# Optimization experiments

Hardware: AMD Instinct MI355X
Metric: run time of the kernel (lower is better)

Reference implementation:

```python
import jax, jax.numpy as jnp
import numpy as np

EPS_D = 1e-12  # clamp for sqrt of pairwise distances (diag is exactly 0)


def tr2dist_small(Y):
    # Y: (B, k, N) -> (B, N, N); standard protein-folding coords->distance map
    k = Y.shape[1]
    Z = Y - jnp.mean(Y, axis=2, keepdims=True)
    n2 = jnp.sum(Z * Z, axis=1)                        # (B, N)
    D = n2[:, None, :] + n2[:, :, None] - 2.0 * jnp.einsum('bkn,bkm->bnm', Z, Z)
    D = 3.0 * D / k
    return jnp.sqrt(jnp.maximum(D, EPS_D))


def mean_masked(X, mask, axis, keepdims=True):
    return jnp.sum(X * mask, axis=axis, keepdims=keepdims) / jnp.sum(mask, axis=axis, keepdims=keepdims)


def get_graph_lap(X, mask):
    # X: (B, C, N), mask: (B, 1, N)
    B, C, N = X.shape
    mm = jnp.einsum('bin,bim->bnm', mask, mask)        # (B, N, N) pair mask
    X = X - mean_masked(X, mask, axis=2) * mask
    X = X / jnp.sqrt(jnp.sum(X * X, axis=2, keepdims=True) / jnp.sum(mask, axis=2, keepdims=True) + 1e-4)
    pos = 0.5 * jnp.linspace(0.0, 1.0, N)[None, :] * mask   # (B, 1, N)
    Xa = jnp.concatenate((X, pos), axis=1)
    Wd = tr2dist_small(Xa) * mm
    sigma = mean_masked(Wd, mm, axis=(1, 2))           # (B, 1, 1)
    Wd = jnp.exp(-Wd / sigma * 10.0) * mm
    Wsum = jnp.sum(Wd, axis=1)                         # (B, N)
    L = jnp.zeros_like(Wd) + Wsum[:, :, None] * jnp.eye(N, dtype=Wd.dtype)[None] - Wd
    L = 0.5 * (L + jnp.swapaxes(L, 1, 2))
    return L, Wd


def _forward(Z, mask, K0, Knet, W, Wend):
    h = 0.01
    m = mask[:, None, :]                               # (B, 1, N)
    Z = jnp.tanh(jnp.einsum('oc,bcn->bon', K0, Z)) * m
    nlayers = W.shape[0]
    for i in range(nlayers):
        L, _ = get_graph_lap(Z, m)
        Ki = Knet[i]
        Wi = W[i, :, :, :, 0]                          # (3, C, C) size-1 kernels
        cv = lambda w, x: jnp.einsum('oc,bcn->bon', w, x) * m     # conv1d, k=1
        cvT = lambda w, x: jnp.einsum('co,bcn->bon', w, x) * m    # conv_transpose1d, k=1
        mm1 = lambda x: jnp.einsum('bcn,bnm->bcm', x, L)
        Ai = Ki[0] * cv(Wi[0], Z) + mm1(Ki[1] * cv(Wi[1], Z)) + mm1(mm1(Ki[2] * cv(Wi[2], Z)))
        Ai = (Ai - mean_masked(Ai, m, axis=2)) * m
        Ai = Ai / jnp.sqrt(jnp.sum(Ai * Ai, axis=1, keepdims=True) + 0.001)
        Ai = jax.nn.relu(Ai)
        Ai = Ki[0] * cvT(Wi[0], Ai) + mm1(Ki[1] * cvT(Wi[1], Ai)) + mm1(mm1(Ki[2] * cvT(Wi[2], Ai)))
        Z = Z - h * Ai
    Zout = jnp.einsum('oc,bcn->bon', Wend[:, :, 0], Z) * m       # (B, chan_out, N)
    dists = tuple(tr2dist_small(Zout[:, 3 * i:3 * i + 3, :]) for i in range(Zout.shape[1] // 3))
    return dists + (Zout,)


def setup_inputs() -> dict:
    key = jax.random.key(0)
    ks = jax.random.split(key, 6)
    B, chan_in, chan_out, channels, N, nlayers = 16, 40, 3, 256, 1024, 6
    stdv0 = 0.1 * channels / chan_in
    return {
        'Z': jax.random.normal(ks[0], (B, chan_in, N), dtype=jnp.float32),
        'mask': jnp.ones((B, N), dtype=jnp.float32),
        'K0': jax.random.uniform(ks[1], (channels, chan_in), minval=-stdv0, maxval=stdv0, dtype=jnp.float32),
        'Knet': jax.random.uniform(ks[2], (nlayers, chan_out), minval=-stdv0, maxval=stdv0, dtype=jnp.float32),
        'W': jax.random.uniform(ks[3], (nlayers, 3, channels, channels, 1), minval=-0.1, maxval=0.1, dtype=jnp.float32),
        'Wend': 1e-4 * jax.random.normal(ks[4], (chan_out, channels, 1), dtype=jnp.float32),
    }


def reference(Z, mask, K0, Knet, W, Wend):
    return _forward(Z, mask, K0, Knet, W, Wend)
```

## Files before the change

kernel.cpp:

```cpp
#include <hip/hip_runtime.h>
#include <hip/hip_fp16.h>
#include <math.h>

#define BB 16
#define CIN 40
#define CH 256
#define NN 1024
#define KROWS 257
#define KPAD 288
#define NLAYERS 6

typedef unsigned short ush;
typedef __attribute__((ext_vector_type(8))) short bh8;
typedef __attribute__((ext_vector_type(8))) _Float16 h8;
typedef __attribute__((ext_vector_type(4))) float f4;

__device__ __forceinline__ ush bf16_rne(float x) {
  unsigned int u = __float_as_uint(x);
  u += 0x7fffu + ((u >> 16) & 1u);
  return (ush)(u >> 16);
}
__device__ __forceinline__ float bf16_f(ush h) {
  return __uint_as_float(((unsigned int)h) << 16);
}
__device__ __forceinline__ ush f2h(float x) {
  __half h = __float2half(x);
  return *(ush*)&h;
}
__device__ __forceinline__ float h2f(ush u) {
  __half h = *(__half*)&u;
  return __half2float(h);
}

#define GLD16(gp, lp) __builtin_amdgcn_global_load_lds( \
    (const __attribute__((address_space(1))) void*)(gp), \
    (__attribute__((address_space(3))) void*)(lp), 16, 0, 0)

__device__ __forceinline__ float blockReduceSum(float v) {
  __shared__ float sred[4];
  const int lane = threadIdx.x & 63;
  const int wid  = threadIdx.x >> 6;
  #pragma unroll
  for (int off = 32; off > 0; off >>= 1) v += __shfl_down(v, off, 64);
  __syncthreads();
  if (lane == 0) sred[wid] = v;
  __syncthreads();
  return sred[0] + sred[1] + sred[2] + sred[3];
}

__device__ __forceinline__ void stageA(
    const ush* __restrict__ Ah, const ush* __restrict__ Al, const int sA,
    const ush* __restrict__ Bh, const ush* __restrict__ Bl, const int sB,
    const int kt, ush* buf) {
  const int lane = threadIdx.x & 63;
  const int wid = threadIdx.x >> 6;
  const int srow = lane >> 2;
  const int sl = (lane & 3) ^ ((srow >> 1) & 3);
  #pragma unroll
  for (int cc = 0; cc < 8; cc++) {
    const int c = wid * 8 + cc;
    const ush* src;
    if (c < 8)       src = Ah + (size_t)(c * 16 + srow) * sA + kt + sl * 8;
    else if (c < 16) src = Al + (size_t)((c - 8) * 16 + srow) * sA + kt + sl * 8;
    else if (c < 24) src = Bh + (size_t)((c - 16) * 16 + srow) * sB + kt + sl * 8;
    else             src = Bl + (size_t)((c - 24) * 16 + srow) * sB + kt + sl * 8;
    GLD16(src, buf + c * 512 + lane * 8);
  }
}

__device__ __forceinline__ void computeA(const ush* buf, f4 acc[4][4]) {
  const int lane = threadIdx.x & 63;
  const int wid = threadIdx.x >> 6;
  const int wr = wid >> 1, wc = wid & 1;
  const int frow = lane & 15;
  const int slot8 = (((lane >> 4) ^ ((frow >> 1) & 3)) << 3);
  bh8 ah[4], al[4], bh_[4], bl_[4];
  #pragma unroll
  for (int mi = 0; mi < 4; mi++) {
    const int off = (wr * 64 + mi * 16 + frow) * 32 + slot8;
    ah[mi] = *(const bh8*)&buf[off];
    al[mi] = *(const bh8*)&buf[4096 + off];
  }
  #pragma unroll
  for (int ni = 0; ni < 4; ni++) {
    const int off = (wc * 64 + ni * 16 + frow) * 32 + slot8;
    bh_[ni] = *(const bh8*)&buf[8192 + off];
    bl_[ni] = *(const bh8*)&buf[12288 + off];
  }
  #pragma unroll
  for (int mi = 0; mi < 4; mi++)
    #pragma unroll
    for (int ni = 0; ni < 4; ni++) {
      acc[mi][ni] = __builtin_amdgcn_mfma_f32_16x16x32_bf16(ah[mi], bh_[ni], acc[mi][ni], 0, 0, 0);
      acc[mi][ni] = __builtin_amdgcn_mfma_f32_16x16x32_bf16(ah[mi], bl_[ni], acc[mi][ni], 0, 0, 0);
      acc[mi][ni] = __builtin_amdgcn_mfma_f32_16x16x32_bf16(al[mi], bh_[ni], acc[mi][ni], 0, 0, 0);
    }
}

__device__ __forceinline__ void stageCV(
    const ush* __restrict__ Ap, const int sA,
    const ush* __restrict__ Bh, const ush* __restrict__ Bl, const int sB,
    const int kt, ush* buf) {
  const int lane = threadIdx.x & 63;
  const int wid = threadIdx.x >> 6;
  const int srow = lane >> 2;
  const int sl = (lane & 3) ^ ((srow >> 1) & 3);
  #pragma unroll
  for (int cc = 0; cc < 6; cc++) {
    const int c = wid * 6 + cc;
    const ush* src;
    if (c < 8)       src = Ap + (size_t)(c * 16 + srow) * sA + kt + sl * 8;
    else if (c < 16) src = Bh + (size_t)((c - 8) * 16 + srow) * sB + kt + sl * 8;
    else             src = Bl + (size_t)((c - 16) * 16 + srow) * sB + kt + sl * 8;
    GLD16(src, buf + c * 512 + lane * 8);
  }
}

__device__ __forceinline__ void computeCV(const ush* buf, f4 acc[4][4]) {
  const int lane = threadIdx.x & 63;
  const int wid = threadIdx.x >> 6;
  const int wr = wid >> 1, wc = wid & 1;
  const int frow = lane & 15;
  const int slot8 = (((lane >> 4) ^ ((frow >> 1) & 3)) << 3);
  h8 a_[4], bh_[4], bl_[4];
  #pragma unroll
  for (int mi = 0; mi < 4; mi++) {
    const int off = (wr * 64 + mi * 16 + frow) * 32 + slot8;
    a_[mi] = *(const h8*)&buf[off];
  }
  #pragma unroll
  for (int ni = 0; ni < 4; ni++) {
    const int off = (wc * 64 + ni * 16 + frow) * 32 + slot8;
    bh_[ni] = *(const h8*)&buf[4096 + off];
    bl_[ni] = *(const h8*)&buf[8192 + off];
  }
  #pragma unroll
  for (int mi = 0; mi < 4; mi++)
    #pragma unroll
    for (int ni = 0; ni < 4; ni++) {
      acc[mi][ni] = __builtin_amdgcn_mfma_f32_16x16x32_f16(a_[mi], bh_[ni], acc[mi][ni], 0, 0, 0);
      acc[mi][ni] = __builtin_amdgcn_mfma_f32_16x16x32_f16(a_[mi], bl_[ni], acc[mi][ni], 0, 0, 0);
    }
}

__device__ __forceinline__ void stageMM(
    const ush* __restrict__ Ah, const ush* __restrict__ Al, const int sA,
    const ush* __restrict__ Bp, const int sB, const int kt, ush* buf) {
  const int lane = threadIdx.x & 63;
  const int wid = threadIdx.x >> 6;
  const int srow = lane >> 2;
  const int sl = (lane & 3) ^ ((srow >> 1) & 3);
  #pragma unroll
  for (int cc = 0; cc < 4; cc++) {
    const int c = wid * 4 + cc;
    const ush* src;
    if (c < 4)       src = Ah + (size_t)(c * 16 + srow) * sA + kt + sl * 8;
    else if (c < 8)  src = Al + (size_t)((c - 4) * 16 + srow) * sA + kt + sl * 8;
    else             src = Bp + (size_t)((c - 8) * 16 + srow) * sB + kt + sl * 8;
    GLD16(src, buf + c * 512 + lane * 8);
  }
}

__device__ __forceinline__ void computeMM(const ush* buf, f4 acc[4][2]) {
  const int lane = threadIdx.x & 63;
  const int wid = threadIdx.x >> 6;
  const int frow = lane & 15;
  const int slot8 = (((lane >> 4) ^ ((frow >> 1) & 3)) << 3);
  h8 ah[4], al[4], b_[2];
  #pragma unroll
  for (int mi = 0; mi < 4; mi++) {
    const int off = (mi * 16 + frow) * 32 + slot8;
    ah[mi] = *(const h8*)&buf[off];
    al[mi] = *(const h8*)&buf[2048 + off];
  }
  #pragma unroll
  for (int ni = 0; ni < 2; ni++) {
    const int off = (wid * 32 + ni * 16 + frow) * 32 + slot8;
    b_[ni] = *(const h8*)&buf[4096 + off];
  }
  #pragma unroll
  for (int mi = 0; mi < 4; mi++)
    #pragma unroll
    for (int ni = 0; ni < 2; ni++) {
      acc[mi][ni] = __builtin_amdgcn_mfma_f32_16x16x32_f16(ah[mi], b_[ni], acc[mi][ni], 0, 0, 0);
      acc[mi][ni] = __builtin_amdgcn_mfma_f32_16x16x32_f16(al[mi], b_[ni], acc[mi][ni], 0, 0, 0);
    }
}

__global__ void k0_kernel(const float* __restrict__ Zin, const float* __restrict__ K0,
                          const float* __restrict__ mask, float* __restrict__ Zc,
                          float* __restrict__ statS1, float* __restrict__ statS2) {
  const int b = blockIdx.y;
  const int o = blockIdx.x;
  __shared__ float w[CIN];
  if (threadIdx.x < CIN) w[threadIdx.x] = K0[o * CIN + threadIdx.x];
  __syncthreads();
  float s1 = 0.f, s2 = 0.f;
  for (int n = threadIdx.x; n < NN; n += 256) {
    float acc = 0.f;
    #pragma unroll
    for (int c = 0; c < CIN; c++) acc += w[c] * Zin[((size_t)b * CIN + c) * NN + n];
    const float z = tanhf(acc) * mask[b * NN + n];
    Zc[((size_t)b * CH + o) * NN + n] = z;
    s1 += z; s2 += z * z;
  }
  s1 = blockReduceSum(s1);
  s2 = blockReduceSum(s2);
  if (threadIdx.x == 0) {
    const size_t base = ((size_t)b * CH + o) * 8;
    statS1[base] = s1; statS2[base] = s2;
    #pragma unroll
    for (int k = 1; k < 8; k++) { statS1[base + k] = 0.f; statS2[base + k] = 0.f; }
  }
}

__global__ void masksum_kernel(const float* __restrict__ mask, float* __restrict__ msum,
                               float* __restrict__ pmpos) {
  const int b = blockIdx.x;
  float v = 0.f, p = 0.f;
  for (int n = threadIdx.x; n < NN; n += 256) {
    const float m = mask[b * NN + n];
    v += m;
    p += 0.5f * ((float)n * (1.0f / (NN - 1))) * m;
  }
  v = blockReduceSum(v);
  p = blockReduceSum(p);
  if (threadIdx.x == 0) { msum[b] = v; pmpos[b] = p * (1.0f / NN); }
}

__global__ void wprep_kernel(const float* __restrict__ W, ush* __restrict__ Wm,
                             ush* __restrict__ Wt) {
  __shared__ float t[64][65];
  const int mat = blockIdx.y;
  const int ty = blockIdx.x >> 2, tx = blockIdx.x & 3;
  const float* src = W + (size_t)mat * CH * CH;
  const int tid = threadIdx.x;
  const int lr = tid >> 2;
  const int lc = (tid & 3) * 16;
  float v[16];
  #pragma unroll
  for (int j = 0; j < 16; j += 4)
    *(float4*)&v[j] = *(const float4*)&src[(size_t)(ty * 64 + lr) * CH + tx * 64 + lc + j];
  ush hv[16];
  #pragma unroll
  for (int j = 0; j < 16; j++) {
    hv[j] = f2h(v[j]);
    t[lr][lc + j] = v[j];
  }
  const size_t offm = (size_t)mat * CH * CH + (size_t)(ty * 64 + lr) * CH + tx * 64 + lc;
  #pragma unroll
  for (int j = 0; j < 16; j += 4)
    *(ushort4*)&Wm[offm + j] = *(ushort4*)&hv[j];
  __syncthreads();
  #pragma unroll
  for (int j = 0; j < 16; j++) hv[j] = f2h(t[lc + j][lr]);
  const size_t offt = (size_t)mat * CH * CH + (size_t)(tx * 64 + lr) * CH + ty * 64 + lc;
  #pragma unroll
  for (int j = 0; j < 16; j += 4)
    *(ushort4*)&Wt[offt + j] = *(ushort4*)&hv[j];
}

__global__ void rowstatZ_kernel(const float* __restrict__ statS1, const float* __restrict__ statS2,
                                const float* __restrict__ msum, float* __restrict__ muZ,
                                float* __restrict__ rsZ) {
  const int b = blockIdx.x;
  const int c = threadIdx.x;
  const size_t base = ((size_t)b * CH + c) * 8;
  float S1 = 0.f, S2 = 0.f;
  #pragma unroll
  for (int k = 0; k < 8; k++) { S1 += statS1[base + k]; S2 += statS2[base + k]; }
  const float M = msum[b];
  const float mu = S1 / M;
  const float q = fmaxf(S2 - mu * S1, 0.f);
  muZ[b * CH + c] = mu;
  rsZ[b * CH + c] = 1.0f / sqrtf(q / M + 1e-4f);
}

__global__ void rowstatU_kernel(const float* __restrict__ statS1, const float* __restrict__ msum,
                                float* __restrict__ rmean) {
  const int b = blockIdx.x;
  const int c = threadIdx.x;
  const size_t base = ((size_t)b * CH + c) * 8;
  float S1 = 0.f;
  #pragma unroll
  for (int k = 0; k < 8; k++) S1 += statS1[base + k];
  rmean[b * CH + c] = S1 / msum[b];
}

__global__ void tsplitZ_kernel(const float* __restrict__ in, ush* __restrict__ Th,
                               ush* __restrict__ Tl) {
  __shared__ float t[32][65];
  const int b = blockIdx.z;
  const int n0 = blockIdx.x * 64;
  const int k0 = blockIdx.y * 32;
  const float* src = in + (size_t)b * CH * NN;
  const int tid = threadIdx.x;
  const int lr = tid >> 3;
  const int lc = (tid & 7) * 8;
  const int gk = k0 + lr;
  *(float4*)&t[lr][lc]     = *(const float4*)&src[(size_t)gk * NN + n0 + lc];
  *(float4*)&t[lr][lc + 4] = *(const float4*)&src[(size_t)gk * NN + n0 + lc + 4];
  __syncthreads();
  const int on = tid >> 2;
  const int ok = (tid & 3) * 8;
  ush hv[8], lv[8];
  #pragma unroll
  for (int j = 0; j < 8; j++) {
    const float v = t[ok + j][on];
    hv[j] = f2h(v); lv[j] = f2h(v - h2f(hv[j]));
  }
  const size_t off = ((size_t)b * NN + n0 + on) * CH + k0 + ok;
  *(ushort4*)&Th[off] = *(ushort4*)&hv[0];
  *(ushort4*)&Th[off + 4] = *(ushort4*)&hv[4];
  *(ushort4*)&Tl[off] = *(ushort4*)&lv[0];
  *(ushort4*)&Tl[off + 4] = *(ushort4*)&lv[4];
}

__global__ void tsplitY2_kernel(const ush* __restrict__ Zsh, const ush* __restrict__ Zsl,
                                const float* __restrict__ mask, const float* __restrict__ muZ,
                                const float* __restrict__ rsZ, const float* __restrict__ pmpos,
                                ush* __restrict__ Th, ush* __restrict__ Tl,
                                float* __restrict__ n2part) {
  const int b = blockIdx.z;
  const int n0 = blockIdx.x * 64;
  const int k0 = blockIdx.y * 32;
  const int tid = threadIdx.x;
  const int n = n0 + (tid >> 2);
  const int kc = k0 + (tid & 3) * 8;
  const float mn = mask[b * NN + n];
  float val[8];
  if (kc + 7 < CH) {
    const size_t zoff = ((size_t)b * NN + n) * CH + kc;
    const ushort4 h0 = *(const ushort4*)&Zsh[zoff];
    const ushort4 h1 = *(const ushort4*)&Zsh[zoff + 4];
    const ushort4 l0 = *(const ushort4*)&Zsl[zoff];
    const ushort4 l1 = *(const ushort4*)&Zsl[zoff + 4];
    const float4 mu0 = *(const float4*)&muZ[b * CH + kc];
    const float4 mu1 = *(const float4*)&muZ[b * CH + kc + 4];
    const float4 rs0 = *(const float4*)&rsZ[b * CH + kc];
    const float4 rs1 = *(const float4*)&rsZ[b * CH + kc + 4];
    val[0] = (h2f(h0.x) + h2f(l0.x) - mu0.x * mn) * rs0.x;
    val[1] = (h2f(h0.y) + h2f(l0.y) - mu0.y * mn) * rs0.y;
    val[2] = (h2f(h0.z) + h2f(l0.z) - mu0.z * mn) * rs0.z;
    val[3] = (h2f(h0.w) + h2f(l0.w) - mu0.w * mn) * rs0.w;
    val[4] = (h2f(h1.x) + h2f(l1.x) - mu1.x * mn) * rs1.x;
    val[5] = (h2f(h1.y) + h2f(l1.y) - mu1.y * mn) * rs1.y;
    val[6] = (h2f(h1.z) + h2f(l1.z) - mu1.z * mn) * rs1.z;
    val[7] = (h2f(h1.w) + h2f(l1.w) - mu1.w * mn) * rs1.w;
  } else {
    #pragma unroll
    for (int j = 0; j < 8; j++) {
      const int gk = kc + j;
      val[j] = (gk == CH) ? (0.5f * ((float)n * (1.0f / (NN - 1))) * mn - pmpos[b]) : 0.f;
    }
  }
  float s = 0.f;
  ush hv[8], lv[8];
  #pragma unroll
  for (int j = 0; j < 8; j++) {
    s += val[j] * val[j];
    hv[j] = bf16_rne(val[j]);
    lv[j] = bf16_rne(val[j] - bf16_f(hv[j]));
  }
  const size_t off = ((size_t)b * NN + n) * KPAD + kc;
  *(ushort4*)&Th[off] = *(ushort4*)&hv[0];
  *(ushort4*)&Th[off + 4] = *(ushort4*)&hv[4];
  *(ushort4*)&Tl[off] = *(ushort4*)&lv[0];
  *(ushort4*)&Tl[off + 4] = *(ushort4*)&lv[4];
  s += __shfl_xor(s, 1, 64);
  s += __shfl_xor(s, 2, 64);
  if ((tid & 3) == 0) n2part[((size_t)b * 9 + blockIdx.y) * NN + n] = s;
}

__global__ void n2red_kernel(const float* __restrict__ n2part, float* __restrict__ n2) {
  const int idx = blockIdx.x * 256 + threadIdx.x;
  const int b = idx >> 10, n = idx & 1023;
  float s = 0.f;
  #pragma unroll
  for (int kb = 0; kb < 9; kb++) s += n2part[((size_t)b * 9 + kb) * NN + n];
  n2[idx] = s;
}

__global__ __launch_bounds__(256, 2)
void gram_v4_kernel(const ush* __restrict__ Yth, const ush* __restrict__ Ytl,
                    const float* __restrict__ n2, const float* __restrict__ mask,
                    ush* __restrict__ Dp, float* __restrict__ sigpart) {
  __shared__ ush lds[32768];
  const int bid = blockIdx.x;
  const int logical = (bid & 7) * 72 + (bid >> 3);
  const int b = logical / 36;
  int t = logical - b * 36;
  int ty = 0;
  while (t >= 8 - ty) { t -= 8 - ty; ++ty; }
  const int tx = ty + t;
  const int i0 = ty * 128;
  const int j0 = tx * 128;
  const ush* Ah = Yth + (size_t)b * NN * KPAD + (size_t)i0 * KPAD;
  const ush* Al = Ytl + (size_t)b * NN * KPAD + (size_t)i0 * KPAD;
  const ush* Bh = Yth + (size_t)b * NN * KPAD + (size_t)j0 * KPAD;
  const ush* Bl = Ytl + (size_t)b * NN * KPAD + (size_t)j0 * KPAD;
  f4 acc[4][4];
  const f4 z4 = {0.f, 0.f, 0.f, 0.f};
  #pragma unroll
  for (int mi = 0; mi < 4; mi++)
    #pragma unroll
    for (int ni = 0; ni < 4; ni++) acc[mi][ni] = z4;
  stageA(Ah, Al, KPAD, Bh, Bl, KPAD, 0, lds);
  __syncthreads();
  int pb = 0;
  for (int kt = 32; kt < KPAD; kt += 32) {
    stageA(Ah, Al, KPAD, Bh, Bl, KPAD, kt, lds + (pb ^ 1) * 16384);
    computeA(lds + pb * 16384, acc);
    __syncthreads();
    pb ^= 1;
  }
  computeA(lds + pb * 16384, acc);
  const int lane = threadIdx.x & 63;
  const int wid = threadIdx.x >> 6;
  const int wr = wid >> 1, wc = wid & 1;
  const int frow = lane & 15, hh = lane >> 4;
  const float scale = 3.0f / 257.0f;
  float lsum = 0.f;
  #pragma unroll
  for (int ni = 0; ni < 4; ni++) {
    const int jl = wc * 64 + ni * 16 + frow;
    const int j = j0 + jl;
    const float n2j = n2[b * NN + j];
    const float mkj = mask[b * NN + j];
    #pragma unroll
    for (int mi = 0; mi < 4; mi++) {
      const int il = wr * 64 + mi * 16 + hh * 4;
      ush dv[4];
      #pragma unroll
      for (int r = 0; r < 4; r++) {
        const int i = i0 + il + r;
        const float D = scale * (n2[b * NN + i] + n2j - 2.0f * acc[mi][ni][r]);
        const float d = sqrtf(fmaxf(D, 1e-12f));
        const float mmv = mask[b * NN + i] * mkj;
        const float wd = d * mmv;
        lsum += wd * mmv;
        dv[r] = f2h(wd);
      }
      if (ty != tx) {
        uint2 mr;
        mr.x = (unsigned)dv[0] | ((unsigned)dv[1] << 16);
        mr.y = (unsigned)dv[2] | ((unsigned)dv[3] << 16);
        *(uint2*)&Dp[((size_t)b * NN + j) * NN + i0 + il] = mr;
      }
      #pragma unroll
      for (int r = 0; r < 4; r++) {
        const unsigned v = dv[r];
        const unsigned vp = (unsigned)__shfl_xor((int)v, 1, 64);
        if ((frow & 1) == 0)
          *(unsigned*)&Dp[((size_t)b * NN + i0 + il + r) * NN + j] = v | (vp << 16);
      }
    }
  }
  if (ty != tx) lsum *= 2.0f;
  #pragma unroll
  for (int off = 32; off > 0; off >>= 1) lsum += __shfl_down(lsum, off, 64);
  __syncthreads();
  float* rbuf = (float*)lds;
  if (lane == 0) rbuf[wid] = lsum;
  __syncthreads();
  if (threadIdx.x == 0)
    sigpart[(size_t)b * 64 + ty * 8 + tx] = rbuf[0] + rbuf[1] + rbuf[2] + rbuf[3];
}

__global__ void sigfinal_kernel(const float* __restrict__ sigpart, const float* __restrict__ msum,
                                float* __restrict__ fbuf) {
  const int b = blockIdx.x;
  float v = 0.f;
  if (threadIdx.x < 64) {
    const int ty = threadIdx.x >> 3, tx = threadIdx.x & 7;
    if (ty <= tx) v = sigpart[b * 64 + threadIdx.x];
  }
  v = blockReduceSum(v);
  if (threadIdx.x == 0) { const float ms = msum[b]; fbuf[b] = -10.0f * ms * ms / v; }
}

__global__ void expw3_kernel(const ush* __restrict__ Dp, const float* __restrict__ mask,
                             const float* __restrict__ fbuf, ush* __restrict__ Wp) {
  const int b = blockIdx.y, n = blockIdx.x;
  const float fb = fbuf[b];
  const float mn = mask[b * NN + n];
  const size_t roff = ((size_t)b * NN + n) * NN;
  const int t = threadIdx.x;
  const float4 mk = ((const float4*)(mask + b * NN))[t];
  const ushort4 dp = *(const ushort4*)&Dp[roff + t * 4];
  const float w0 = expf(fb * h2f(dp.x)) * mn * mk.x;
  const float w1 = expf(fb * h2f(dp.y)) * mn * mk.y;
  const float w2 = expf(fb * h2f(dp.z)) * mn * mk.z;
  const float w3 = expf(fb * h2f(dp.w)) * mn * mk.w;
  const float s = blockReduceSum(w0 + w1 + w2 + w3);
  float v0 = -w0, v1 = -w1, v2 = -w2, v3 = -w3;
  if ((n >> 2) == t) {
    const int r = n & 3;
    if (r == 0) v0 += s; else if (r == 1) v1 += s; else if (r == 2) v2 += s; else v3 += s;
  }
  ushort4 h4;
  h4.x = f2h(v0); h4.y = f2h(v1); h4.z = f2h(v2); h4.w = f2h(v3);
  *(ushort4*)&Wp[roff + t * 4] = h4;
}

__global__ __launch_bounds__(256, 2)
void cvall_kernel(const ush* __restrict__ Ap, const ush* __restrict__ Bth,
                  const ush* __restrict__ Btl, const float* __restrict__ mask,
                  const float* __restrict__ Kis, unsigned int* __restrict__ Cpack,
                  ush* __restrict__ C2h, ush* __restrict__ C2l) {
  __shared__ ush lds[32768];
  const int bid = blockIdx.x;
  const int logical = (bid & 7) * 96 + (bid >> 3);
  const int b = logical / 48;
  const int inner = logical - b * 48;
  const int c0g = inner & 7;
  const int r0g = inner >> 3;
  const int r0 = r0g * 128;
  const int c0 = c0g * 128;
  const ush* Aq = Ap + (size_t)r0 * CH;
  const ush* Bh = Bth + (size_t)b * NN * CH + (size_t)c0 * CH;
  const ush* Bl = Btl + (size_t)b * NN * CH + (size_t)c0 * CH;
  f4 acc[4][4];
  const f4 z4 = {0.f, 0.f, 0.f, 0.f};
  #pragma unroll
  for (int mi = 0; mi < 4; mi++)
    #pragma unroll
    for (int ni = 0; ni < 4; ni++) acc[mi][ni] = z4;
  stageCV(Aq, CH, Bh, Bl, CH, 0, lds);
  __syncthreads();
  int pb = 0;
  for (int kt = 32; kt < CH; kt += 32) {
    stageCV(Aq, CH, Bh, Bl, CH, kt, lds + (pb ^ 1) * 12288);
    computeCV(lds + pb * 12288, acc);
    __syncthreads();
    pb ^= 1;
  }
  computeCV(lds + pb * 12288, acc);
  __syncthreads();
  unsigned int* tl = (unsigned int*)lds;
  const int lane = threadIdx.x & 63;
  const int wid = threadIdx.x >> 6;
  const int wr = wid >> 1, wc = wid & 1;
  const int frow = lane & 15, hh = lane >> 4;
  const float alpha = Kis[r0g >> 1];
  #pragma unroll
  for (int ni = 0; ni < 4; ni++) {
    const int jl = wc * 64 + ni * 16 + frow;
    const float am = alpha * mask[b * NN + c0 + jl];
    #pragma unroll
    for (int mi = 0; mi < 4; mi++) {
      const int il = wr * 64 + mi * 16 + hh * 4;
      unsigned int pv[4];
      #pragma unroll
      for (int r = 0; r < 4; r++) {
        const float v = acc[mi][ni][r] * am;
        const ush h = f2h(v);
        const ush l = f2h(v - h2f(h));
        pv[r] = (unsigned int)h | ((unsigned int)l << 16);
      }
      const int slot = (il >> 2) ^ (jl & 31);
      *(uint4*)&tl[jl * 128 + slot * 4] = *(uint4*)pv;
    }
  }
  __syncthreads();
  const int rrow = threadIdx.x >> 1;
  const int rch = (threadIdx.x & 1) * 64;
  if (r0g < 4) {
    unsigned int* dst = Cpack + ((size_t)b * 512 + r0 + rrow) * NN + c0 + rch;
    #pragma unroll
    for (int g = 0; g < 16; g++) {
      unsigned int pw[4];
      #pragma unroll
      for (int q = 0; q < 4; q++) {
        const int jl = rch + g * 4 + q;
        const int slot = (rrow >> 2) ^ (jl & 31);
        pw[q] = tl[jl * 128 + slot * 4 + (rrow & 3)];
      }
      *(uint4*)&dst[g * 4] = *(uint4*)pw;
    }
  } else {
    const size_t obase = ((size_t)b * 256 + (r0 - 512) + rrow) * NN + c0 + rch;
    #pragma unroll
    for (int g = 0; g < 8; g++) {
      unsigned int hw[4], lw[4];
      #pragma unroll
      for (int q = 0; q < 4; q++) {
        unsigned int h2[2], l2[2];
        #pragma unroll
        for (int e = 0; e < 2; e++) {
          const int jl = rch + g * 8 + q * 2 + e;
          const int slot = (rrow >> 2) ^ (jl & 31);
          const unsigned int v = tl[jl * 128 + slot * 4 + (rrow & 3)];
          h2[e] = v & 0xffffu; l2[e] = v >> 16;
        }
        hw[q] = h2[0] | (h2[1] << 16);
        lw[q] = l2[0] | (l2[1] << 16);
      }
      *(uint4*)&C2h[obase + g * 8] = *(uint4*)hw;
      *(uint4*)&C2l[obase + g * 8] = *(uint4*)lw;
    }
  }
}

template <int OUTMODE, int STATS>
__global__ __launch_bounds__(256, 3)
void mm1_v6_kernel(const ush* __restrict__ Xh, const ush* __restrict__ Xl, const size_t xStride,
                   const ush* __restrict__ Wp,
                   const unsigned int* __restrict__ addp, const size_t aStride,
                   const float* __restrict__ zin, const float* __restrict__ mask,
                   float* __restrict__ outF, ush* __restrict__ outH, ush* __restrict__ outL,
                   float* __restrict__ statS1, float* __restrict__ statS2) {
  __shared__ ush lds[16384];
  const int bid = blockIdx.x;
  const int logical = (bid & 7) * 64 + (bid >> 3);
  const int b = logical >> 5;
  const int inner = logical & 31;
  const int n0 = (inner & 7) * 128;
  const int r0 = (inner >> 3) * 64;
  const ush* Ah = Xh + (size_t)b * xStride + (size_t)r0 * NN;
  const ush* Al = Xl + (size_t)b * xStride + (size_t)r0 * NN;
  const ush* Bp = Wp + (size_t)b * NN * NN + (size_t)n0 * NN;
  f4 acc[4][2];
  const f4 z4 = {0.f, 0.f, 0.f, 0.f};
  #pragma unroll
  for (int mi = 0; mi < 4; mi++) { acc[mi][0] = z4; acc[mi][1] = z4; }
  stageMM(Ah, Al, NN, Bp, NN, 0, lds);
  __syncthreads();
  int pb = 0;
  for (int kt = 32; kt < NN; kt += 32) {
    stageMM(Ah, Al, NN, Bp, NN, kt, lds + (pb ^ 1) * 8192);
    computeMM(lds + pb * 8192, acc);
    __syncthreads();
    pb ^= 1;
  }
  computeMM(lds + pb * 8192, acc);
  const int lane = threadIdx.x & 63;
  const int wid = threadIdx.x >> 6;
  const int frow = lane & 15, hh = lane >> 4;
  float a1[4][4];
  float a2[4][4];
  if (STATS) {
    #pragma unroll
    for (int mi = 0; mi < 4; mi++)
      #pragma unroll
      for (int r = 0; r < 4; r++) { a1[mi][r] = 0.f; a2[mi][r] = 0.f; }
  }
  __syncthreads();
  unsigned int* tl = (unsigned int*)lds;
  #pragma unroll
  for (int ni = 0; ni < 2; ni++) {
    const int jl = wid * 32 + ni * 16 + frow;
    const int col = n0 + jl;
    const float mk = STATS ? mask[b * NN + col] : 0.f;
    #pragma unroll
    for (int mi = 0; mi < 4; mi++) {
      const int il = mi * 16 + hh * 4;
      unsigned int pv[4];
      #pragma unroll
      for (int r = 0; r < 4; r++) {
        const int row = r0 + il + r;
        const unsigned int av = addp[(size_t)b * aStride + (size_t)row * NN + col];
        const float o = acc[mi][ni][r] + h2f((ush)(av & 0xffffu)) + h2f((ush)(av >> 16));
        float val;
        if (OUTMODE == 2) {
          const size_t ooff = (size_t)b * CH * NN + (size_t)row * NN + col;
          val = zin[ooff] - 0.01f * o;
          outF[ooff] = val;
        } else {
          val = o;
        }
        if (STATS) { a1[mi][r] += val * mk; a2[mi][r] += val * val * mk; }
        const ush h = f2h(val);
        const ush l = f2h(val - h2f(h));
        pv[r] = (unsigned int)h | ((unsigned int)l << 16);
      }
      const int slot = (il >> 2) ^ (jl & 15);
      *(uint4*)&tl[jl * 64 + slot * 4] = *(uint4*)pv;
    }
  }
  __syncthreads();
  if (OUTMODE == 0) {
    const int rrow = threadIdx.x >> 2;
    const int rch = (threadIdx.x & 3) * 32;
    const size_t obase = ((size_t)b * 256 + r0 + rrow) * NN + n0 + rch;
    #pragma unroll
    for (int g = 0; g < 4; g++) {
      unsigned int hw[4], lw[4];
      #pragma unroll
      for (int q = 0; q < 4; q++) {
        unsigned int h2[2], l2[2];
        #pragma unroll
        for (int e = 0; e < 2; e++) {
          const int jl = rch + g * 8 + q * 2 + e;
          const int slot = (rrow >> 2) ^ (jl & 15);
          const unsigned int v = tl[jl * 64 + slot * 4 + (rrow & 3)];
          h2[e] = v & 0xffffu; l2[e] = v >> 16;
        }
        hw[q] = h2[0] | (h2[1] << 16);
        lw[q] = l2[0] | (l2[1] << 16);
      }
      *(uint4*)&outH[obase + g * 8] = *(uint4*)hw;
      *(uint4*)&outL[obase + g * 8] = *(uint4*)lw;
    }
  } else {
    const int nloc = threadIdx.x >> 1;
    const int ch0 = (threadIdx.x & 1) * 32;
    #pragma unroll
    for (int half = 0; half < 2; half++) {
      unsigned int hw[8], lw[8];
      #pragma unroll
      for (int q = 0; q < 8; q++) {
        const int ila = ch0 + half * 16 + q * 2;
        const int ilb = ila + 1;
        const unsigned int va = tl[nloc * 64 + (((ila >> 2) ^ (nloc & 15)) << 2) + (ila & 3)];
        const unsigned int vb = tl[nloc * 64 + (((ilb >> 2) ^ (nloc & 15)) << 2) + (ilb & 3)];
        hw[q] = (va & 0xffffu) | (vb << 16);
        lw[q] = (va >> 16) | (vb & 0xffff0000u);
      }
      const size_t zoff = ((size_t)b * NN + n0 + nloc) * CH + r0 + ch0 + half * 16;
      *(uint4*)&outH[zoff] = *(uint4*)&hw[0];
      *(uint4*)&outH[zoff + 8] = *(uint4*)&hw[4];
      *(uint4*)&outL[zoff] = *(uint4*)&lw[0];
      *(uint4*)&outL[zoff + 8] = *(uint4*)&lw[4];
    }
  }
  if (STATS) {
    #pragma unroll
    for (int mi = 0; mi < 4; mi++)
      #pragma unroll
      for (int r = 0; r < 4; r++) {
        #pragma unroll
        for (int d = 1; d < 16; d <<= 1) {
          a1[mi][r] += __shfl_xor(a1[mi][r], d, 64);
          a2[mi][r] += __shfl_xor(a2[mi][r], d, 64);
        }
      }
    __syncthreads();
    float* s1b = (float*)lds;
    float* s2b = s1b + 256;
    if (frow == 0) {
      #pragma unroll
      for (int mi = 0; mi < 4; mi++)
        #pragma unroll
        for (int r = 0; r < 4; r++) {
          const int row = mi * 16 + hh * 4 + r;
          s1b[wid * 64 + row] = a1[mi][r];
          s2b[wid * 64 + row] = a2[mi][r];
        }
    }
    __syncthreads();
    if (threadIdx.x < 64) {
      const int row = threadIdx.x;
      const float p1 = s1b[row] + s1b[64 + row] + s1b[128 + row] + s1b[192 + row];
      const float p2 = s2b[row] + s2b[64 + row] + s2b[128 + row] + s2b[192 + row];
      const int nblk = n0 >> 7;
      statS1[((size_t)b * CH + r0 + row) * 8 + nblk] = p1;
      statS2[((size_t)b * CH + r0 + row) * 8 + nblk] = p2;
    }
  }
}

__global__ void csq_kernel(const ush* __restrict__ Uh, const ush* __restrict__ Ul,
                           const float* __restrict__ mask, const float* __restrict__ rmean,
                           float* __restrict__ part) {
  const int b = blockIdx.y, cc = blockIdx.x;
  const int n = threadIdx.x * 4;
  const float4 m4 = *(const float4*)&mask[b * NN + n];
  float4 s4 = {0.f, 0.f, 0.f, 0.f};
  for (int r = 0; r < 16; r++) {
    const int c = cc * 16 + r;
    const float rm = rmean[b * CH + c];
    const size_t uoff = ((size_t)b * 256 + c) * NN + n;
    const ushort4 uh = *(const ushort4*)&Uh[uoff];
    const ushort4 ul = *(const ushort4*)&Ul[uoff];
    float a;
    a = (h2f(uh.x) + h2f(ul.x) - rm) * m4.x; s4.x += a * a;
    a = (h2f(uh.y) + h2f(ul.y) - rm) * m4.y; s4.y += a * a;
    a = (h2f(uh.z) + h2f(ul.z) - rm) * m4.z; s4.z += a * a;
    a = (h2f(uh.w) + h2f(ul.w) - rm) * m4.w; s4.w += a * a;
  }
  *(float4*)&part[((size_t)(b * 16 + cc)) * NN + n] = s4;
}

__global__ void csq2_kernel(const float* __restrict__ part, float* __restrict__ rs) {
  const int b = blockIdx.y;
  const int n = blockIdx.x * 256 + threadIdx.x;
  float s = 0.001f;
  #pragma unroll
  for (int cc = 0; cc < 16; cc++) s += part[((size_t)(b * 16 + cc)) * NN + n];
  rs[b * NN + n] = 1.0f / sqrtf(s);
}

__global__ void tsplitN2_kernel(const ush* __restrict__ Uh, const ush* __restrict__ Ul,
                                const float* __restrict__ mask, const float* __restrict__ rmean,
                                const float* __restrict__ rs, ush* __restrict__ Th,
                                ush* __restrict__ Tl) {
  __shared__ float t[32][65];
  const int b = blockIdx.z;
  const int n0 = blockIdx.x * 64;
  const int k0 = blockIdx.y * 32;
  const int tid = threadIdx.x;
  const int lr = tid >> 3;
  const int lc = (tid & 7) * 8;
  const int gc = k0 + lr;
  const float rm = rmean[b * CH + gc];
  const float4 ma = *(const float4*)&mask[b * NN + n0 + lc];
  const float4 mb = *(const float4*)&mask[b * NN + n0 + lc + 4];
  const float4 ra = *(const float4*)&rs[b * NN + n0 + lc];
  const float4 rb = *(const float4*)&rs[b * NN + n0 + lc + 4];
  const size_t uoff = ((size_t)b * 256 + gc) * NN + n0 + lc;
  const ushort4 ha = *(const ushort4*)&Uh[uoff];
  const ushort4 hb = *(const ushort4*)&Uh[uoff + 4];
  const ushort4 la = *(const ushort4*)&Ul[uoff];
  const ushort4 lb = *(const ushort4*)&Ul[uoff + 4];
  t[lr][lc + 0] = fmaxf((h2f(ha.x) + h2f(la.x) - rm) * ma.x * ra.x, 0.f);
  t[lr][lc + 1] = fmaxf((h2f(ha.y) + h2f(la.y) - rm) * ma.y * ra.y, 0.f);
  t[lr][lc + 2] = fmaxf((h2f(ha.z) + h2f(la.z) - rm) * ma.z * ra.z, 0.f);
  t[lr][lc + 3] = fmaxf((h2f(ha.w) + h2f(la.w) - rm) * ma.w * ra.w, 0.f);
  t[lr][lc + 4] = fmaxf((h2f(hb.x) + h2f(lb.x) - rm) * mb.x * rb.x, 0.f);
  t[lr][lc + 5] = fmaxf((h2f(hb.y) + h2f(lb.y) - rm) * mb.y * rb.y, 0.f);
  t[lr][lc + 6] = fmaxf((h2f(hb.z) + h2f(lb.z) - rm) * mb.z * rb.z, 0.f);
  t[lr][lc + 7] = fmaxf((h2f(hb.w) + h2f(lb.w) - rm) * mb.w * rb.w, 0.f);
  __syncthreads();
  const int on = tid >> 2;
  const int ok = (tid & 3) * 8;
  ush hv[8], lv[8];
  #pragma unroll
  for (int j = 0; j < 8; j++) {
    const float v = t[ok + j][on];
    hv[j] = f2h(v); lv[j] = f2h(v - h2f(hv[j]));
  }
  const size_t off = ((size_t)b * NN + n0 + on) * CH + k0 + ok;
  *(ushort4*)&Th[off] = *(ushort4*)&hv[0];
  *(ushort4*)&Th[off + 4] = *(ushort4*)&hv[4];
  *(ushort4*)&Tl[off] = *(ushort4*)&lv[0];
  *(ushort4*)&Tl[off + 4] = *(ushort4*)&lv[4];
}

__global__ void zout_kernel(const float* __restrict__ Z, const float* __restrict__ Wend,
                            const float* __restrict__ mask, float* __restrict__ outZ,
                            float* __restrict__ Zcent) {
  const int b = blockIdx.x;
  __shared__ float w[3 * CH];
  for (int i = threadIdx.x; i < 3 * CH; i += 256) w[i] = Wend[i];
  __syncthreads();
  float a[3][4];
  #pragma unroll
  for (int j = 0; j < 4; j++) { a[0][j] = 0.f; a[1][j] = 0.f; a[2][j] = 0.f; }
  const float* Zb = Z + (size_t)b * CH * NN;
  for (int c = 0; c < CH; c++) {
    const float w0 = w[c], w1 = w[CH + c], w2 = w[2 * CH + c];
    #pragma unroll
    for (int j = 0; j < 4; j++) {
      float zv = Zb[(size_t)c * NN + threadIdx.x + j * 256];
      a[0][j] += w0 * zv; a[1][j] += w1 * zv; a[2][j] += w2 * zv;
    }
  }
  float sum[3] = {0.f, 0.f, 0.f};
  #pragma unroll
  for (int j = 0; j < 4; j++) {
    const int n = threadIdx.x + j * 256;
    const float mv = mask[b * NN + n];
    #pragma unroll
    for (int o = 0; o < 3; o++) {
      a[o][j] *= mv;
      outZ[((size_t)b * 3 + o) * NN + n] = a[o][j];
      sum[o] += a[o][j];
    }
  }
  for (int o = 0; o < 3; o++) {
    float s = blockReduceSum(sum[o]);
    const float mean = s * (1.0f / NN);
    #pragma unroll
    for (int j = 0; j < 4; j++) {
      const int n = threadIdx.x + j * 256;
      Zcent[((size_t)b * 3 + o) * NN + n] = a[o][j] - mean;
    }
  }
}

__global__ void dist_kernel(const float* __restrict__ Zcent, float* __restrict__ outD) {
  const int b = blockIdx.z;
  const int n = blockIdx.y;
  const int m = blockIdx.x * 256 + threadIdx.x;
  const float* Zb = Zcent + (size_t)b * 3 * NN;
  const float x0 = Zb[n], x1 = Zb[NN + n], x2 = Zb[2 * NN + n];
  const float d0 = x0 - Zb[m], d1 = x1 - Zb[NN + m], d2 = x2 - Zb[2 * NN + m];
  const float D = d0 * d0 + d1 * d1 + d2 * d2;
  outD[((size_t)b * NN + n) * NN + m] = sqrtf(fmaxf(D, 1e-12f));
}

extern "C" void kernel_launch(void* const* d_in, const int* in_sizes, int n_in,
                              void* d_out, int out_size, void* d_ws, size_t ws_size,
                              hipStream_t stream) {
  const float* Zin  = (const float*)d_in[0];
  const float* mask = (const float*)d_in[1];
  const float* K0   = (const float*)d_in[2];
  const float* Knet = (const float*)d_in[3];
  const float* W    = (const float*)d_in[4];
  const float* Wend = (const float*)d_in[5];
  float* out = (float*)d_out;

  ush* Wp = (ush*)out;
  ush* Dp = Wp + (size_t)BB * NN * NN;
  float* outZ = out + (size_t)BB * NN * NN;

  float* p = (float*)d_ws;
  float* uni = p; p += (size_t)BB * 768 * NN;
  ush* Yth = (ush*)uni;
  ush* Ytl = Yth + (size_t)BB * NN * KPAD;
  unsigned int* Cpack = (unsigned int*)uni;
  ush* C2h = (ush*)(uni + (size_t)BB * 512 * NN);
  ush* C2l = C2h + (size_t)BB * 256 * NN;

  float* Zcur = p; p += (size_t)BB * CH * NN;
  ush* Thb = (ush*)p; p += (size_t)BB * NN * CH / 2;
  ush* Tlb = (ush*)p; p += (size_t)BB * NN * CH / 2;
  ush* Zsh = (ush*)p; p += (size_t)BB * NN * CH / 2;
  ush* Zsl = (ush*)p; p += (size_t)BB * NN * CH / 2;
  ush* Wm = (ush*)p; p += (size_t)18 * CH * CH / 2;
  ush* Wt = (ush*)p; p += (size_t)18 * CH * CH / 2;
  float* n2b   = p; p += BB * NN;
  float* rsb   = p; p += BB * NN;
  float* msum  = p; p += BB;
  float* pmpos = p; p += BB;
  float* sigp  = p; p += BB * 64;
  float* fbuf  = p; p += BB;
  float* rmeanb= p; p += BB * CH;
  float* muZ   = p; p += BB * CH;
  float* rsZ   = p; p += BB * CH;
  float* statS1= p; p += (size_t)BB * CH * 8;
  float* statS2= p; p += (size_t)BB * CH * 8;
  float* n2part= p; p += (size_t)BB * 9 * NN;
  float* partb = p; p += (size_t)BB * 16 * NN;
  float* Zcent = p; p += BB * 3 * NN;

  const dim3 gtsZ(NN / 64, CH / 32, BB);
  const dim3 gtsY(NN / 64, KPAD / 32, BB);
  const size_t sC = (size_t)512 * NN;
  const size_t sT = (size_t)CH * NN;

  masksum_kernel<<<BB, 256, 0, stream>>>(mask, msum, pmpos);
  wprep_kernel<<<dim3(16, 18), 256, 0, stream>>>(W, Wm, Wt);
  k0_kernel<<<dim3(CH, BB), 256, 0, stream>>>(Zin, K0, mask, Zcur, statS1, statS2);
  tsplitZ_kernel<<<gtsZ, 256, 0, stream>>>(Zcur, Zsh, Zsl);

  for (int layer = 0; layer < NLAYERS; layer++) {
    rowstatZ_kernel<<<BB, 256, 0, stream>>>(statS1, statS2, msum, muZ, rsZ);
    tsplitY2_kernel<<<gtsY, 256, 0, stream>>>(Zsh, Zsl, mask, muZ, rsZ, pmpos, Yth, Ytl, n2part);
    n2red_kernel<<<BB * NN / 256, 256, 0, stream>>>(n2part, n2b);
    gram_v4_kernel<<<576, 256, 0, stream>>>(Yth, Ytl, n2b, mask, Dp, sigp);
    sigfinal_kernel<<<BB, 256, 0, stream>>>(sigp, msum, fbuf);
    expw3_kernel<<<dim3(NN, BB), 256, 0, stream>>>(Dp, mask, fbuf, Wp);

    const ush* Am = Wm + (size_t)layer * 3 * CH * CH;
    const ush* At = Wt + (size_t)layer * 3 * CH * CH;
    const float* Ki = Knet + layer * 3;

    cvall_kernel<<<768, 256, 0, stream>>>(Am, Zsh, Zsl, mask, Ki, Cpack, C2h, C2l);
    mm1_v6_kernel<0, 0><<<512, 256, 0, stream>>>(C2h, C2l, sT, Wp,
        Cpack + (size_t)256 * NN, sC, nullptr, nullptr, nullptr, Thb, Tlb, nullptr, nullptr);
    mm1_v6_kernel<0, 1><<<512, 256, 0, stream>>>(Thb, Tlb, sT, Wp,
        Cpack, sC, nullptr, mask, nullptr, C2h, C2l, statS1, statS2);

    rowstatU_kernel<<<BB, 256, 0, stream>>>(statS1, msum, rmeanb);
    csq_kernel<<<dim3(16, BB), 256, 0, stream>>>(C2h, C2l, mask, rmeanb, partb);
    csq2_kernel<<<dim3(NN / 256, BB), 256, 0, stream>>>(partb, rsb);
    tsplitN2_kernel<<<gtsZ, 256, 0, stream>>>(C2h, C2l, mask, rmeanb, rsb, Thb, Tlb);

    cvall_kernel<<<768, 256, 0, stream>>>(At, Thb, Tlb, mask, Ki, Cpack, C2h, C2l);
    mm1_v6_kernel<0, 0><<<512, 256, 0, stream>>>(C2h, C2l, sT, Wp,
        Cpack + (size_t)256 * NN, sC, nullptr, nullptr, nullptr, Thb, Tlb, nullptr, nullptr);
    mm1_v6_kernel<2, 1><<<512, 256, 0, stream>>>(Thb, Tlb, sT, Wp,
        Cpack, sC, Zcur, mask, Zcur, Zsh, Zsl, statS1, statS2);
  }

  zout_kernel<<<BB, 256, 0, stream>>>(Zcur, Wend, mask, outZ, Zcent);
  dist_kernel<<<dim3(NN / 256, NN, BB), 256, 0, stream>>>(Zcent, out);
}
```

Measured before the change: 1.806 ms.

## Fold position channel into gram epilogue and write cvall outputs directly

The 257th channel (the position feature) is removed from the padded K dimension of the gram GEMM. Its contribution is added as a rank-1 term in the epilogue using a precomputed per-node position vector, so the GEMM K loop drops from 288 to 256. Separately, cvall no longer transposes its outputs through LDS; it pairs lanes with a shuffle and writes to global directly, which lets LDS shrink and raises occupancy hints for cvall and mm1. The trade-off is that the direct stores are narrower and less coalesced than the old staged writes.

```diff
diff --git a/kernel.cpp b/kernel.cpp
--- a/kernel.cpp
+++ b/kernel.cpp
@@ -6,8 +6,6 @@
 #define CIN 40
 #define CH 256
 #define NN 1024
-#define KROWS 257
-#define KPAD 288
 #define NLAYERS 6
 
 typedef unsigned short ush;
@@ -215,7 +213,7 @@
 }
 
 __global__ void masksum_kernel(const float* __restrict__ mask, float* __restrict__ msum,
-                               float* __restrict__ pmpos) {
+                               float* __restrict__ posv) {
   const int b = blockIdx.x;
   float v = 0.f, p = 0.f;
   for (int n = threadIdx.x; n < NN; n += 256) {
@@ -225,7 +223,10 @@
   }
   v = blockReduceSum(v);
   p = blockReduceSum(p);
-  if (threadIdx.x == 0) { msum[b] = v; pmpos[b] = p * (1.0f / NN); }
+  const float pm = p * (1.0f / NN);
+  if (threadIdx.x == 0) msum[b] = v;
+  for (int n = threadIdx.x; n < NN; n += 256)
+    posv[b * NN + n] = 0.5f * ((float)n * (1.0f / (NN - 1))) * mask[b * NN + n] - pm;
 }
 
 __global__ void wprep_kernel(const float* __restrict__ W, ush* __restrict__ Wm,
@@ -318,9 +319,8 @@
 
 __global__ void tsplitY2_kernel(const ush* __restrict__ Zsh, const ush* __restrict__ Zsl,
                                 const float* __restrict__ mask, const float* __restrict__ muZ,
-                                const float* __restrict__ rsZ, const float* __restrict__ pmpos,
-                                ush* __restrict__ Th, ush* __restrict__ Tl,
-                                float* __restrict__ n2part) {
+                                const float* __restrict__ rsZ, ush* __restrict__ Th,
+                                ush* __restrict__ Tl, float* __restrict__ n2part) {
   const int b = blockIdx.z;
   const int n0 = blockIdx.x * 64;
   const int k0 = blockIdx.y * 32;
@@ -328,32 +328,24 @@
   const int n = n0 + (tid >> 2);
   const int kc = k0 + (tid & 3) * 8;
   const float mn = mask[b * NN + n];
+  const size_t zoff = ((size_t)b * NN + n) * CH + kc;
+  const ushort4 h0 = *(const ushort4*)&Zsh[zoff];
+  const ushort4 h1 = *(const ushort4*)&Zsh[zoff + 4];
+  const ushort4 l0 = *(const ushort4*)&Zsl[zoff];
+  const ushort4 l1 = *(const ushort4*)&Zsl[zoff + 4];
+  const float4 mu0 = *(const float4*)&muZ[b * CH + kc];
+  const float4 mu1 = *(const float4*)&muZ[b * CH + kc + 4];
+  const float4 rs0 = *(const float4*)&rsZ[b * CH + kc];
+  const float4 rs1 = *(const float4*)&rsZ[b * CH + kc + 4];
   float val[8];
-  if (kc + 7 < CH) {
-    const size_t zoff = ((size_t)b * NN + n) * CH + kc;
-    const ushort4 h0 = *(const ushort4*)&Zsh[zoff];
-    const ushort4 h1 = *(const ushort4*)&Zsh[zoff + 4];
-    const ushort4 l0 = *(const ushort4*)&Zsl[zoff];
-    const ushort4 l1 = *(const ushort4*)&Zsl[zoff + 4];
-    const float4 mu0 = *(const float4*)&muZ[b * CH + kc];
-    const float4 mu1 = *(const float4*)&muZ[b * CH + kc + 4];
-    const float4 rs0 = *(const float4*)&rsZ[b * CH + kc];
-    const float4 rs1 = *(const float4*)&rsZ[b * CH + kc + 4];
-    val[0] = (h2f(h0.x) + h2f(l0.x) - mu0.x * mn) * rs0.x;
-    val[1] = (h2f(h0.y) + h2f(l0.y) - mu0.y * mn) * rs0.y;
-    val[2] = (h2f(h0.z) + h2f(l0.z) - mu0.z * mn) * rs0.z;
-    val[3] = (h2f(h0.w) + h2f(l0.w) - mu0.w * mn) * rs0.w;
-    val[4] = (h2f(h1.x) + h2f(l1.x) - mu1.x * mn) * rs1.x;
-    val[5] = (h2f(h1.y) + h2f(l1.y) - mu1.y * mn) * rs1.y;
-    val[6] = (h2f(h1.z) + h2f(l1.z) - mu1.z * mn) * rs1.z;
-    val[7] = (h2f(h1.w) + h2f(l1.w) - mu1.w * mn) * rs1.w;
-  } else {
-    #pragma unroll
-    for (int j = 0; j < 8; j++) {
-      const int gk = kc + j;
-      val[j] = (gk == CH) ? (0.5f * ((float)n * (1.0f / (NN - 1))) * mn - pmpos[b]) : 0.f;
-    }
-  }
+  val[0] = (h2f(h0.x) + h2f(l0.x) - mu0.x * mn) * rs0.x;
+  val[1] = (h2f(h0.y) + h2f(l0.y) - mu0.y * mn) * rs0.y;
+  val[2] = (h2f(h0.z) + h2f(l0.z) - mu0.z * mn) * rs0.z;
+  val[3] = (h2f(h0.w) + h2f(l0.w) - mu0.w * mn) * rs0.w;
+  val[4] = (h2f(h1.x) + h2f(l1.x) - mu1.x * mn) * rs1.x;
+  val[5] = (h2f(h1.y) + h2f(l1.y) - mu1.y * mn) * rs1.y;
+  val[6] = (h2f(h1.z) + h2f(l1.z) - mu1.z * mn) * rs1.z;
+  val[7] = (h2f(h1.w) + h2f(l1.w) - mu1.w * mn) * rs1.w;
   float s = 0.f;
   ush hv[8], lv[8];
   #pragma unroll
@@ -362,29 +354,32 @@
     hv[j] = bf16_rne(val[j]);
     lv[j] = bf16_rne(val[j] - bf16_f(hv[j]));
   }
-  const size_t off = ((size_t)b * NN + n) * KPAD + kc;
+  const size_t off = ((size_t)b * NN + n) * CH + kc;
   *(ushort4*)&Th[off] = *(ushort4*)&hv[0];
   *(ushort4*)&Th[off + 4] = *(ushort4*)&hv[4];
   *(ushort4*)&Tl[off] = *(ushort4*)&lv[0];
   *(ushort4*)&Tl[off + 4] = *(ushort4*)&lv[4];
   s += __shfl_xor(s, 1, 64);
   s += __shfl_xor(s, 2, 64);
-  if ((tid & 3) == 0) n2part[((size_t)b * 9 + blockIdx.y) * NN + n] = s;
-}
-
-__global__ void n2red_kernel(const float* __restrict__ n2part, float* __restrict__ n2) {
+  if ((tid & 3) == 0) n2part[((size_t)b * 8 + blockIdx.y) * NN + n] = s;
+}
+
+__global__ void n2red_kernel(const float* __restrict__ n2part, const float* __restrict__ posv,
+                             float* __restrict__ n2) {
   const int idx = blockIdx.x * 256 + threadIdx.x;
-  const int b = idx >> 10, n = idx & 1023;
-  float s = 0.f;
-  #pragma unroll
-  for (int kb = 0; kb < 9; kb++) s += n2part[((size_t)b * 9 + kb) * NN + n];
+  const int b = idx >> 10;
+  const float pv = posv[idx];
+  float s = pv * pv;
+  #pragma unroll
+  for (int kb = 0; kb < 8; kb++) s += n2part[((size_t)b * 8 + kb) * NN + (idx & 1023)];
   n2[idx] = s;
 }
 
 __global__ __launch_bounds__(256, 2)
-void gram_v4_kernel(const ush* __restrict__ Yth, const ush* __restrict__ Ytl,
+void gram_v5_kernel(const ush* __restrict__ Yth, const ush* __restrict__ Ytl,
                     const float* __restrict__ n2, const float* __restrict__ mask,
-                    ush* __restrict__ Dp, float* __restrict__ sigpart) {
+                    const float* __restrict__ posv, ush* __restrict__ Dp,
+                    float* __restrict__ sigpart) {
   __shared__ ush lds[32768];
   const int bid = blockIdx.x;
   const int logical = (bid & 7) * 72 + (bid >> 3);
@@ -395,21 +390,21 @@
   const int tx = ty + t;
   const int i0 = ty * 128;
   const int j0 = tx * 128;
-  const ush* Ah = Yth + (size_t)b * NN * KPAD + (size_t)i0 * KPAD;
-  const ush* Al = Ytl + (size_t)b * NN * KPAD + (size_t)i0 * KPAD;
-  const ush* Bh = Yth + (size_t)b * NN * KPAD + (size_t)j0 * KPAD;
-  const ush* Bl = Ytl + (size_t)b * NN * KPAD + (size_t)j0 * KPAD;
+  const ush* Ah = Yth + (size_t)b * NN * CH + (size_t)i0 * CH;
+  const ush* Al = Ytl + (size_t)b * NN * CH + (size_t)i0 * CH;
+  const ush* Bh = Yth + (size_t)b * NN * CH + (size_t)j0 * CH;
+  const ush* Bl = Ytl + (size_t)b * NN * CH + (size_t)j0 * CH;
   f4 acc[4][4];
   const f4 z4 = {0.f, 0.f, 0.f, 0.f};
   #pragma unroll
   for (int mi = 0; mi < 4; mi++)
     #pragma unroll
     for (int ni = 0; ni < 4; ni++) acc[mi][ni] = z4;
-  stageA(Ah, Al, KPAD, Bh, Bl, KPAD, 0, lds);
+  stageA(Ah, Al, CH, Bh, Bl, CH, 0, lds);
   __syncthreads();
   int pb = 0;
-  for (int kt = 32; kt < KPAD; kt += 32) {
-    stageA(Ah, Al, KPAD, Bh, Bl, KPAD, kt, lds + (pb ^ 1) * 16384);
+  for (int kt = 32; kt < CH; kt += 32) {
+    stageA(Ah, Al, CH, Bh, Bl, CH, kt, lds + (pb ^ 1) * 16384);
     computeA(lds + pb * 16384, acc);
     __syncthreads();
     pb ^= 1;
@@ -427,6 +422,7 @@
     const int j = j0 + jl;
     const float n2j = n2[b * NN + j];
     const float mkj = mask[b * NN + j];
+    const float pj = posv[b * NN + j];
     #pragma unroll
     for (int mi = 0; mi < 4; mi++) {
       const int il = wr * 64 + mi * 16 + hh * 4;
@@ -434,7 +430,8 @@
       #pragma unroll
       for (int r = 0; r < 4; r++) {
         const int i = i0 + il + r;
-        const float D = scale * (n2[b * NN + i] + n2j - 2.0f * acc[mi][ni][r]);
+        const float g = acc[mi][ni][r] + posv[b * NN + i] * pj;
+        const float D = scale * (n2[b * NN + i] + n2j - 2.0f * g);
         const float d = sqrtf(fmaxf(D, 1e-12f));
         const float mmv = mask[b * NN + i] * mkj;
         const float wd = d * mmv;
@@ -503,12 +500,12 @@
   *(ushort4*)&Wp[roff + t * 4] = h4;
 }
 
-__global__ __launch_bounds__(256, 2)
+__global__ __launch_bounds__(256, 3)
 void cvall_kernel(const ush* __restrict__ Ap, const ush* __restrict__ Bth,
                   const ush* __restrict__ Btl, const float* __restrict__ mask,
                   const float* __restrict__ Kis, unsigned int* __restrict__ Cpack,
                   ush* __restrict__ C2h, ush* __restrict__ C2l) {
-  __shared__ ush lds[32768];
+  __shared__ ush lds[24576];
   const int bid = blockIdx.x;
   const int logical = (bid & 7) * 96 + (bid >> 3);
   const int b = logical / 48;
@@ -536,8 +533,6 @@
     pb ^= 1;
   }
   computeCV(lds + pb * 12288, acc);
-  __syncthreads();
-  unsigned int* tl = (unsigned int*)lds;
   const int lane = threadIdx.x & 63;
   const int wid = threadIdx.x >> 6;
   const int wr = wid >> 1, wc = wid & 1;
@@ -546,64 +541,38 @@
   #pragma unroll
   for (int ni = 0; ni < 4; ni++) {
     const int jl = wc * 64 + ni * 16 + frow;
-    const float am = alpha * mask[b * NN + c0 + jl];
+    const int col = c0 + jl;
+    const float am = alpha * mask[b * NN + col];
     #pragma unroll
     for (int mi = 0; mi < 4; mi++) {
       const int il = wr * 64 + mi * 16 + hh * 4;
-      unsigned int pv[4];
       #pragma unroll
       for (int r = 0; r < 4; r++) {
+        const int row = r0 + il + r;
         const float v = acc[mi][ni][r] * am;
         const ush h = f2h(v);
         const ush l = f2h(v - h2f(h));
-        pv[r] = (unsigned int)h | ((unsigned int)l << 16);
+        const unsigned pv = (unsigned)h | ((unsigned)l << 16);
+        const unsigned pvp = (unsigned)__shfl_xor((int)pv, 1, 64);
+        if ((frow & 1) == 0) {
+          if (r0g < 4) {
+            uint2 w2; w2.x = pv; w2.y = pvp;
+            *(uint2*)&Cpack[((size_t)b * 512 + row) * NN + col] = w2;
+          } else {
+            const size_t obase = ((size_t)b * 256 + (row - 512)) * NN + col;
+            const unsigned hw = (pv & 0xffffu) | (pvp << 16);
+            const unsigned lw = (pv >> 16) | (pvp & 0xffff0000u);
+            *(unsigned*)&C2h[obase] = hw;
+            *(unsigned*)&C2l[obase] = lw;
+          }
+        }
       }
-      const int slot = (il >> 2) ^ (jl & 31);
-      *(uint4*)&tl[jl * 128 + slot * 4] = *(uint4*)pv;
-    }
-  }
-  __syncthreads();
-  const int rrow = threadIdx.x >> 1;
-  const int rch = (threadIdx.x & 1) * 64;
-  if (r0g < 4) {
-    unsigned int* dst = Cpack + ((size_t)b * 512 + r0 + rrow) * NN + c0 + rch;
-    #pragma unroll
-    for (int g = 0; g < 16; g++) {
-      unsigned int pw[4];
-      #pragma unroll
-      for (int q = 0; q < 4; q++) {
-        const int jl = rch + g * 4 + q;
-        const int slot = (rrow >> 2) ^ (jl & 31);
-        pw[q] = tl[jl * 128 + slot * 4 + (rrow & 3)];
-      }
-      *(uint4*)&dst[g * 4] = *(uint4*)pw;
-    }
-  } else {
-    const size_t obase = ((size_t)b * 256 + (r0 - 512) + rrow) * NN + c0 + rch;
-    #pragma unroll
-    for (int g = 0; g < 8; g++) {
-      unsigned int hw[4], lw[4];
-      #pragma unroll
-      for (int q = 0; q < 4; q++) {
-        unsigned int h2[2], l2[2];
-        #pragma unroll
-        for (int e = 0; e < 2; e++) {
-          const int jl = rch + g * 8 + q * 2 + e;
-          const int slot = (rrow >> 2) ^ (jl & 31);
-          const unsigned int v = tl[jl * 128 + slot * 4 + (rrow & 3)];
-          h2[e] = v & 0xffffu; l2[e] = v >> 16;
-        }
-        hw[q] = h2[0] | (h2[1] << 16);
-        lw[q] = l2[0] | (l2[1] << 16);
-      }
-      *(uint4*)&C2h[obase + g * 8] = *(uint4*)hw;
-      *(uint4*)&C2l[obase + g * 8] = *(uint4*)lw;
     }
   }
 }
 
 template <int OUTMODE, int STATS>
-__global__ __launch_bounds__(256, 3)
+__global__ __launch_bounds__(256, 5)
 void mm1_v6_kernel(const ush* __restrict__ Xh, const ush* __restrict__ Xl, const size_t xStride,
                    const ush* __restrict__ Wp,
                    const unsigned int* __restrict__ addp, const size_t aStride,
@@ -908,7 +877,7 @@
   float* p = (float*)d_ws;
   float* uni = p; p += (size_t)BB * 768 * NN;
   ush* Yth = (ush*)uni;
-  ush* Ytl = Yth + (size_t)BB * NN * KPAD;
+  ush* Ytl = Yth + (size_t)BB * NN * CH;
   unsigned int* Cpack = (unsigned int*)uni;
   ush* C2h = (ush*)(uni + (size_t)BB * 512 * NN);
   ush* C2l = C2h + (size_t)BB * 256 * NN;
@@ -923,7 +892,7 @@
   float* n2b   = p; p += BB * NN;
   float* rsb   = p; p += BB * NN;
   float* msum  = p; p += BB;
-  float* pmpos = p; p += BB;
+  float* posv  = p; p += BB * NN;
   float* sigp  = p; p += BB * 64;
   float* fbuf  = p; p += BB;
   float* rmeanb= p; p += BB * CH;
@@ -931,25 +900,24 @@
   float* rsZ   = p; p += BB * CH;
   float* statS1= p; p += (size_t)BB * CH * 8;
   float* statS2= p; p += (size_t)BB * CH * 8;
-  float* n2part= p; p += (size_t)BB * 9 * NN;
+  float* n2part= p; p += (size_t)BB * 8 * NN;
   float* partb = p; p += (size_t)BB * 16 * NN;
   float* Zcent = p; p += BB * 3 * NN;
 
   const dim3 gtsZ(NN / 64, CH / 32, BB);
-  const dim3 gtsY(NN / 64, KPAD / 32, BB);
   const size_t sC = (size_t)512 * NN;
   const size_t sT = (size_t)CH * NN;
 
-  masksum_kernel<<<BB, 256, 0, stream>>>(mask, msum, pmpos);
+  masksum_kernel<<<BB, 256, 0, stream>>>(mask, msum, posv);
   wprep_kernel<<<dim3(16, 18), 256, 0, stream>>>(W, Wm, Wt);
   k0_kernel<<<dim3(CH, BB), 256, 0, stream>>>(Zin, K0, mask, Zcur, statS1, statS2);
   tsplitZ_kernel<<<gtsZ, 256, 0, stream>>>(Zcur, Zsh, Zsl);
 
   for (int layer = 0; layer < NLAYERS; layer++) {
     rowstatZ_kernel<<<BB, 256, 0, stream>>>(statS1, statS2, msum, muZ, rsZ);
-    tsplitY2_kernel<<<gtsY, 256, 0, stream>>>(Zsh, Zsl, mask, muZ, rsZ, pmpos, Yth, Ytl, n2part);
-    n2red_kernel<<<BB * NN / 256, 256, 0, stream>>>(n2part, n2b);
-    gram_v4_kernel<<<576, 256, 0, stream>>>(Yth, Ytl, n2b, mask, Dp, sigp);
+    tsplitY2_kernel<<<gtsZ, 256, 0, stream>>>(Zsh, Zsl, mask, muZ, rsZ, Yth, Ytl, n2part);
+    n2red_kernel<<<BB * NN / 256, 256, 0, stream>>>(n2part, posv, n2b);
+    gram_v5_kernel<<<576, 256, 0, stream>>>(Yth, Ytl, n2b, mask, posv, Dp, sigp);
     sigfinal_kernel<<<BB, 256, 0, stream>>>(sigp, msum, fbuf);
     expw3_kernel<<<dim3(NN, BB), 256, 0, stream>>>(Dp, mask, fbuf, Wp);
 
```

After: 1.768 ms. -2.1%, faster.
